# Performance work log

Hardware: AMD Instinct MI355X
Metric: run time of the kernel (lower is better)

Reference implementation:

```python
import jax, jax.numpy as jnp
import numpy as np

ATT_HEAD = 12
IN_DIM = 768
OUT_DIM = IN_DIM // ATT_HEAD
LEAKY_ALPHA = 0.2
B, N = 8, 512


def setup_inputs() -> dict:
    key = jax.random.key(0)
    ks = jax.random.split(key, 8)
    feat_in = jax.random.normal(ks[0], (B, N, IN_DIM), dtype=jnp.float32)
    adj = jax.random.randint(ks[1], (B, N, N), 0, 2) > 0
    # xavier_uniform for W: fan_in=in_dim, fan_out=out_dim
    lim_W = float(np.sqrt(6.0 / (IN_DIM + OUT_DIM)))
    W = jax.random.uniform(ks[2], (ATT_HEAD, IN_DIM, OUT_DIM), minval=-lim_W, maxval=lim_W, dtype=jnp.float32)
    b = jnp.zeros((OUT_DIM,), dtype=jnp.float32)
    lim_w = float(np.sqrt(6.0 / (OUT_DIM + 1)))
    w_src = jax.random.uniform(ks[3], (ATT_HEAD, OUT_DIM, 1), minval=-lim_w, maxval=lim_w, dtype=jnp.float32)
    w_dst = jax.random.uniform(ks[4], (ATT_HEAD, OUT_DIM, 1), minval=-lim_w, maxval=lim_w, dtype=jnp.float32)
    # xavier_normal for H.weight [in_dim, in_dim]
    std_H = float(np.sqrt(2.0 / (IN_DIM + IN_DIM)))
    H_w = jax.random.normal(ks[5], (IN_DIM, IN_DIM), dtype=jnp.float32) * std_H
    H_b = jax.random.normal(ks[6], (IN_DIM,), dtype=jnp.float32) * 0.01
    return {"feat_in": feat_in, "adj": adj, "W": W, "b": b,
            "w_src": w_src, "w_dst": w_dst, "H_w": H_w, "H_b": H_b}


def reference(feat_in, adj, W, b, w_src, w_dst, H_w, H_b):
    # h: [B, heads, N, out_dim]
    h = jnp.einsum('bnd,ade->bane', feat_in, W)
    th = jnp.tanh(h)
    attn_src = jnp.einsum('bane,aeo->bano', th, w_src)  # [B,A,N,1]
    attn_dst = jnp.einsum('bane,aeo->bano', th, w_dst)  # [B,A,N,1]
    attn = attn_src + jnp.swapaxes(attn_dst, 2, 3)      # [B,A,N,N]
    attn = jnp.where(attn >= 0, attn, LEAKY_ALPHA * attn)
    mask = ~adj[:, None, :, :]                           # [B,1,N,N]
    attn = jnp.where(mask, jnp.float32(-999.0), attn)
    attn = jax.nn.softmax(attn, axis=-1)
    feat_out = jnp.einsum('banm,bame->bane', attn, h) + b
    feat_out = jnp.swapaxes(feat_out, 1, 2).reshape(feat_in.shape[0], feat_in.shape[1], -1)
    feat_out = jax.nn.elu(feat_out)
    gate = jax.nn.sigmoid(feat_in @ H_w.T + H_b)
    return gate * feat_out + (1.0 - gate) * feat_in
```

## Files before the change

kernel.cpp:

```cpp
#include <hip/hip_runtime.h>
#include <hip/hip_bf16.h>

#define BB 8
#define NN 512
#define AH 12
#define DIN 768
#define EE 64
#define MM (BB*NN)
#define YY (BB*AH)
#define LEAKY 0.2f

typedef unsigned short u16;
typedef unsigned int u32;
typedef __attribute__((ext_vector_type(8))) short short8;
typedef __attribute__((ext_vector_type(4))) float f32x4;

static __device__ __forceinline__ u16 f2bf(float f) {
    u32 u = __builtin_bit_cast(u32, f);
    u32 r = (u + 0x7FFFu + ((u >> 16) & 1u)) >> 16;
    return (u16)r;
}
static __device__ __forceinline__ u32 pk2(float a, float b) {
    return (u32)f2bf(a) | ((u32)f2bf(b) << 16);
}
static __device__ __forceinline__ float ftanh(float x) {
    x = fminf(fmaxf(x, -15.f), 15.f);
    return 1.f - 2.f / (__expf(2.f * x) + 1.f);
}
static __device__ __forceinline__ void gl_lds16(const u16* g, u16* l) {
    __builtin_amdgcn_global_load_lds((const __attribute__((address_space(1))) unsigned int*)g,
                                     (__attribute__((address_space(3))) unsigned int*)l,
                                     16, 0, 0);
}

static __device__ __forceinline__ void mfma_probe(int lane, int* prow, int* pcol) {
    int q = lane >> 4, x = lane & 15;
    short8 af, bf;
#pragma unroll
    for (int j = 0; j < 8; j++) {
        int k = q * 8 + j;
        af[j] = (short)f2bf((k < 16) ? (float)(x * 16 + k) : 0.f);
        bf[j] = (short)f2bf((k == x) ? 1.f : 0.f);
    }
    f32x4 d = {};
    d = __builtin_amdgcn_mfma_f32_16x16x32_bf16(af, bf, d, 0, 0, 0);
#pragma unroll
    for (int r = 0; r < 4; r++) {
        int v = (int)(d[r] + 0.5f);
        prow[r] = v >> 4;
        pcol[r] = v & 15;
    }
}

__global__ __launch_bounds__(256) void pack_adj_kernel(const int* __restrict__ adj,
                                                       u32* __restrict__ maskbuf) {
    int t = threadIdx.x, w = t >> 6, ln = t & 63;
    int row = blockIdx.x * 4 + w;
    const int* ar = adj + (size_t)row * NN;
#pragma unroll
    for (int it = 0; it < 8; it++) {
        unsigned long long bal = __ballot(ar[it * 64 + ln] != 0);
        if (ln == 0) {
            maskbuf[row * 16 + it * 2]     = (u32)bal;
            maskbuf[row * 16 + it * 2 + 1] = (u32)(bal >> 32);
        }
    }
}

#define N_FEAT (MM*DIN)
#define N_W    (AH*DIN*EE)
__global__ __launch_bounds__(256) void convert_kernel(const float* __restrict__ feat,
                                                      const float* __restrict__ W,
                                                      const float* __restrict__ Hw,
                                                      u16* __restrict__ featb,
                                                      u16* __restrict__ Wt,
                                                      u16* __restrict__ Hwb) {
    int i = blockIdx.x * 256 + threadIdx.x;
    if (i < N_FEAT) { featb[i] = f2bf(feat[i]); return; }
    int i2 = i - N_FEAT;
    if (i2 < N_W) {
        int a = i2 / (DIN * EE), rem = i2 % (DIN * EE);
        int e = rem / DIN, d = rem % DIN;
        Wt[i2] = f2bf(W[a * (DIN * EE) + d * EE + e]);
        return;
    }
    int i3 = i2 - N_W;
    Hwb[i3] = f2bf(Hw[i3]);
}

#define GEMM_CORE(Abase, Bbase)                                               \
    int wm = w & 1, wn = w >> 1, xr = x & 7;                                  \
    int srow = t >> 3;                                                        \
    int skoff = ((t & 7) ^ (srow & 7)) * 8;                                   \
    const u16* Agp = (Abase) + srow * DIN + skoff;                            \
    const u16* Bgp = (Bbase) + srow * DIN + skoff;                            \
    u16* Asw = As + w * 512;                                                  \
    u16* Bsw = Bs + w * 512;                                                  \
    const u16* ApA = As + (wm * 32 + x) * 64;                                 \
    const u16* ApB = Bs + (wn * 32 + x) * 64;                                 \
    f32x4 acc00 = {}, acc01 = {}, acc10 = {}, acc11 = {};                     \
    for (int k0 = 0; k0 < DIN; k0 += 64) {                                    \
        gl_lds16(Agp + k0, Asw);                                              \
        gl_lds16(Agp + 32 * DIN + k0, Asw + 2048);                            \
        gl_lds16(Bgp + k0, Bsw);                                              \
        gl_lds16(Bgp + 32 * DIN + k0, Bsw + 2048);                            \
        __syncthreads();                                                      \
        _Pragma("unroll")                                                     \
        for (int kk = 0; kk < 2; kk++) {                                      \
            int c8 = ((q + kk * 4) ^ xr) * 8;                                 \
            short8 a0 = *(const short8*)(ApA + c8);                           \
            short8 a1 = *(const short8*)(ApA + 16 * 64 + c8);                 \
            short8 b0 = *(const short8*)(ApB + c8);                           \
            short8 b1 = *(const short8*)(ApB + 16 * 64 + c8);                 \
            acc00 = __builtin_amdgcn_mfma_f32_16x16x32_bf16(a0, b0, acc00, 0, 0, 0); \
            acc01 = __builtin_amdgcn_mfma_f32_16x16x32_bf16(a0, b1, acc01, 0, 0, 0); \
            acc10 = __builtin_amdgcn_mfma_f32_16x16x32_bf16(a1, b0, acc10, 0, 0, 0); \
            acc11 = __builtin_amdgcn_mfma_f32_16x16x32_bf16(a1, b1, acc11, 0, 0, 0); \
        }                                                                     \
        __syncthreads();                                                      \
    }                                                                         \
    int prow[4], pcol[4];                                                     \
    mfma_probe(lane, prow, pcol);                                             \
    _Pragma("unroll")                                                         \
    for (int r = 0; r < 4; r++) {                                             \
        cs[wm * 32 + prow[r]][wn * 32 + pcol[r]]           = acc00[r];        \
        cs[wm * 32 + prow[r]][wn * 32 + 16 + pcol[r]]      = acc01[r];        \
        cs[wm * 32 + 16 + prow[r]][wn * 32 + pcol[r]]      = acc10[r];        \
        cs[wm * 32 + 16 + prow[r]][wn * 32 + 16 + pcol[r]] = acc11[r];        \
    }                                                                         \
    __syncthreads();

__global__ __launch_bounds__(256) void gemm_h_kernel(const u16* __restrict__ featb,
                                                     const u16* __restrict__ Wt,
                                                     const float* __restrict__ wsrc,
                                                     const float* __restrict__ wdst,
                                                     u16* __restrict__ hT,
                                                     float* __restrict__ Sbuf,
                                                     float* __restrict__ Dbuf) {
    __shared__ u16 As[64 * 64];
    __shared__ u16 Bs[64 * 64];
    __shared__ alignas(16) float cs[64][68];
    int t = threadIdx.x, w = t >> 6, lane = t & 63, q = lane >> 4, x = lane & 15;
    int m0 = blockIdx.x * 64, a = blockIdx.y;

    GEMM_CORE(featb + (size_t)m0 * DIN, Wt + (size_t)a * EE * DIN)

    int b = m0 >> 9;
    int y = b * AH + a;
    int nbase = m0 & 511;

    {
        int e = t >> 2, ng = t & 3;
        u32* dst = (u32*)&hT[((size_t)y * EE + e) * NN + nbase + ng * 16];
#pragma unroll
        for (int i = 0; i < 8; i++)
            dst[i] = pk2(cs[ng * 16 + 2 * i][e], cs[ng * 16 + 2 * i + 1][e]);
    }
    {
        int r = t >> 2, cg = t & 3;
        float s = 0.f, d = 0.f;
#pragma unroll
        for (int i = 0; i < 16; i++) {
            int e2 = cg * 16 + i;
            float th = ftanh(cs[r][e2]);
            s += th * wsrc[a * EE + e2];
            d += th * wdst[a * EE + e2];
        }
        s += __shfl_xor(s, 1); s += __shfl_xor(s, 2);
        d += __shfl_xor(d, 1); d += __shfl_xor(d, 2);
        if (cg == 0) {
            Sbuf[y * NN + nbase + r] = s;
            Dbuf[y * NN + nbase + r] = d;
        }
    }
}

static __device__ __forceinline__ float sigm(float z) {
    z = fminf(fmaxf(z, -80.f), 80.f);
    return 1.f / (1.f + __expf(-z));
}
__global__ __launch_bounds__(256) void gemm_gate_kernel(const u16* __restrict__ featb,
                                                        const u16* __restrict__ Hwb,
                                                        const float* __restrict__ Hb,
                                                        const float* __restrict__ feat,
                                                        float* __restrict__ out) {
    __shared__ u16 As[64 * 64];
    __shared__ u16 Bs[64 * 64];
    __shared__ alignas(16) float cs[64][68];
    int t = threadIdx.x, w = t >> 6, lane = t & 63, q = lane >> 4, x = lane & 15;
    int m0 = blockIdx.x * 64, n0 = blockIdx.y * 64;

    GEMM_CORE(featb + (size_t)m0 * DIN, Hwb + (size_t)n0 * DIN)

    float4 hb = *(const float4*)&Hb[n0 + (t & 15) * 4];
#pragma unroll
    for (int p = 0; p < 4; p++) {
        int ml = p * 16 + (t >> 4), c4 = (t & 15) * 4;
        float4 v4 = *(const float4*)&cs[ml][c4];
        size_t idx = (size_t)(m0 + ml) * DIN + n0 + c4;
        float4 fo = *(const float4*)&out[idx];
        float4 f4 = *(const float4*)&feat[idx];
        float4 o;
        float g;
        g = sigm(v4.x + hb.x); o.x = g * fo.x + (1.f - g) * f4.x;
        g = sigm(v4.y + hb.y); o.y = g * fo.y + (1.f - g) * f4.y;
        g = sigm(v4.z + hb.z); o.z = g * fo.z + (1.f - g) * f4.z;
        g = sigm(v4.w + hb.w); o.w = g * fo.w + (1.f - g) * f4.w;
        *(float4*)&out[idx] = o;
    }
}

__global__ __launch_bounds__(256) void attn_kernel(const u16* __restrict__ hT,
                                                   const float* __restrict__ Sbuf,
                                                   const float* __restrict__ Dbuf,
                                                   const u32* __restrict__ maskbuf,
                                                   const float* __restrict__ bias,
                                                   float* __restrict__ out) {
    __shared__ alignas(16) float sdst[NN];
    __shared__ u32 smask[64][17];
    __shared__ float silv[64];
    __shared__ alignas(16) float cs[64][68];

    int t = threadIdx.x;
    int y = blockIdx.y, bb = y / AH, a = y % AH;
    int i0 = blockIdx.x * 64;

    sdst[t] = Dbuf[y * NN + t];
    sdst[t + 256] = Dbuf[y * NN + 256 + t];
#pragma unroll
    for (int p = 0; p < 4; p++) {
        int idx = p * 256 + t, r = idx >> 4, c = idx & 15;
        smask[r][c] = maskbuf[((bb << 9) + i0 + r) * 16 + c];
    }
    __syncthreads();

    int w = t >> 6, lane = t & 63, q = lane >> 4, x = lane & 15;
    int rowl = w * 16 + x;
    float srcv = Sbuf[y * NN + i0 + rowl];

    u32 anym = 0;
#pragma unroll
    for (int c = 0; c < 16; c++) anym |= smask[rowl][c];
    int uni = (anym == 0);

    const u16* hTy = hT + (size_t)y * EE * NN;
    f32x4 acc[4] = {};
    float lsum = 0.f;

#pragma unroll 2
    for (int k0 = 0; k0 < NN; k0 += 32) {
        u32 mb = smask[rowl][k0 >> 5] >> (q * 8);
        float pv[8];
#pragma unroll
        for (int j = 0; j < 8; j++) {
            float v = srcv + sdst[k0 + q * 8 + j];
            v = fmaxf(v, LEAKY * v);
            float e = __expf(fminf(v, 60.f));
            float pm = ((mb >> j) & 1) ? e : 0.f;
            pv[j] = uni ? 1.0f : pm;
            lsum += pv[j];
        }
        short8 af;
        af[0] = (short)f2bf(pv[0]); af[1] = (short)f2bf(pv[1]);
        af[2] = (short)f2bf(pv[2]); af[3] = (short)f2bf(pv[3]);
        af[4] = (short)f2bf(pv[4]); af[5] = (short)f2bf(pv[5]);
        af[6] = (short)f2bf(pv[6]); af[7] = (short)f2bf(pv[7]);
        const u16* hp = hTy + (size_t)x * NN + k0 + q * 8;
        short8 b0 = *(const short8*)(hp);
        short8 b1 = *(const short8*)(hp + 16 * NN);
        short8 b2 = *(const short8*)(hp + 32 * NN);
        short8 b3 = *(const short8*)(hp + 48 * NN);
        acc[0] = __builtin_amdgcn_mfma_f32_16x16x32_bf16(af, b0, acc[0], 0, 0, 0);
        acc[1] = __builtin_amdgcn_mfma_f32_16x16x32_bf16(af, b1, acc[1], 0, 0, 0);
        acc[2] = __builtin_amdgcn_mfma_f32_16x16x32_bf16(af, b2, acc[2], 0, 0, 0);
        acc[3] = __builtin_amdgcn_mfma_f32_16x16x32_bf16(af, b3, acc[3], 0, 0, 0);
    }

    lsum += __shfl_xor(lsum, 16);
    lsum += __shfl_xor(lsum, 32);
    if (q == 0) silv[rowl] = 1.f / fmaxf(lsum, 1e-30f);

    int prow[4], pcol[4];
    mfma_probe(lane, prow, pcol);
#pragma unroll
    for (int nt = 0; nt < 4; nt++)
#pragma unroll
        for (int r = 0; r < 4; r++)
            cs[w * 16 + prow[r]][nt * 16 + pcol[r]] = acc[nt][r];
    __syncthreads();

    float4 b4 = *(const float4*)&bias[(t & 15) * 4];
#pragma unroll
    for (int p = 0; p < 4; p++) {
        int nl = p * 16 + (t >> 4), e4 = (t & 15) * 4;
        float il = silv[nl];
        float4 c4 = *(const float4*)&cs[nl][e4];
        float4 o;
        float v;
        v = c4.x * il + b4.x; o.x = v > 0.f ? v : __expf(v) - 1.f;
        v = c4.y * il + b4.y; o.y = v > 0.f ? v : __expf(v) - 1.f;
        v = c4.z * il + b4.z; o.z = v > 0.f ? v : __expf(v) - 1.f;
        v = c4.w * il + b4.w; o.w = v > 0.f ? v : __expf(v) - 1.f;
        *(float4*)&out[((size_t)(bb << 9) + i0 + nl) * DIN + a * EE + e4] = o;
    }
}

extern "C" void kernel_launch(void* const* d_in, const int* in_sizes, int n_in,
                              void* d_out, int out_size, void* d_ws, size_t ws_size,
                              hipStream_t stream) {
    const float* feat  = (const float*)d_in[0];
    const int*   adj   = (const int*)  d_in[1];
    const float* W     = (const float*)d_in[2];
    const float* bvec  = (const float*)d_in[3];
    const float* wsrc  = (const float*)d_in[4];
    const float* wdst  = (const float*)d_in[5];
    const float* Hw    = (const float*)d_in[6];
    const float* Hb    = (const float*)d_in[7];
    float* out = (float*)d_out;

    char* ws = (char*)d_ws;
    u16*  featb   = (u16*)(ws);
    u16*  Wt      = (u16*)(ws + 6291456);
    u16*  Hwb     = (u16*)(ws + 7471104);
    u16*  hT      = (u16*)(ws + 8650752);
    float* Sbuf   = (float*)(ws + 14942208);
    float* Dbuf   = (float*)(ws + 15138816);
    u32*  maskbuf = (u32*)(ws + 15335424);

    pack_adj_kernel<<<MM / 4, 256, 0, stream>>>(adj, maskbuf);
    convert_kernel<<<(N_FEAT + 2 * N_W) / 256, 256, 0, stream>>>(feat, W, Hw, featb, Wt, Hwb);
    gemm_h_kernel<<<dim3(MM / 64, AH), 256, 0, stream>>>(featb, Wt, wsrc, wdst, hT, Sbuf, Dbuf);
    attn_kernel<<<dim3(NN / 64, YY), 256, 0, stream>>>(hT, Sbuf, Dbuf, maskbuf, bvec, out);
    gemm_gate_kernel<<<dim3(MM / 64, DIN / 64), 256, 0, stream>>>(featb, Hwb, Hb, feat, out);
}
```

Measured before the change: 145.3 us.

## Precompute exp factors for leaky-relu softmax and fuse gating into attention epilogue

The src and dst scores are now exponentiated once in the projection kernel as exp(s) and exp(0.2s) pairs. The attention inner loop then forms each weight as a product of two factors, choosing the leaky branch by testing whether the product reaches 1, so no exp is needed per element. BF16 packing of the probabilities switches from rounding to truncation. The gate GEMM now writes sigmoid values to a buffer, and the attention epilogue applies the gated blend with feat, which removes one read-modify-write pass over out. The costs are an extra gate buffer round-trip, clamping of scores to ±40 which can overflow or lose precision for large values, and truncation error in the probabilities.

```diff
diff --git a/kernel.cpp b/kernel.cpp
--- a/kernel.cpp
+++ b/kernel.cpp
@@ -14,6 +14,7 @@
 typedef unsigned int u32;
 typedef __attribute__((ext_vector_type(8))) short short8;
 typedef __attribute__((ext_vector_type(4))) float f32x4;
+typedef __attribute__((ext_vector_type(4))) u32 u32x4;
 
 static __device__ __forceinline__ u16 f2bf(float f) {
     u32 u = __builtin_bit_cast(u32, f);
@@ -22,6 +23,9 @@
 }
 static __device__ __forceinline__ u32 pk2(float a, float b) {
     return (u32)f2bf(a) | ((u32)f2bf(b) << 16);
+}
+static __device__ __forceinline__ u32 pk2t(float a, float b) {
+    return (__builtin_bit_cast(u32, a) >> 16) | (__builtin_bit_cast(u32, b) & 0xFFFF0000u);
 }
 static __device__ __forceinline__ float ftanh(float x) {
     x = fminf(fmaxf(x, -15.f), 15.f);
@@ -135,8 +139,8 @@
                                                      const float* __restrict__ wsrc,
                                                      const float* __restrict__ wdst,
                                                      u16* __restrict__ hT,
-                                                     float* __restrict__ Sbuf,
-                                                     float* __restrict__ Dbuf) {
+                                                     float2* __restrict__ Spair,
+                                                     float2* __restrict__ Dpair) {
     __shared__ u16 As[64 * 64];
     __shared__ u16 Bs[64 * 64];
     __shared__ alignas(16) float cs[64][68];
@@ -169,8 +173,10 @@
         s += __shfl_xor(s, 1); s += __shfl_xor(s, 2);
         d += __shfl_xor(d, 1); d += __shfl_xor(d, 2);
         if (cg == 0) {
-            Sbuf[y * NN + nbase + r] = s;
-            Dbuf[y * NN + nbase + r] = d;
+            s = fminf(fmaxf(s, -40.f), 40.f);
+            d = fminf(fmaxf(d, -40.f), 40.f);
+            Spair[y * NN + nbase + r] = make_float2(__expf(s), __expf(0.2f * s));
+            Dpair[y * NN + nbase + r] = make_float2(__expf(d), __expf(0.2f * d));
         }
     }
 }
@@ -182,8 +188,7 @@
 __global__ __launch_bounds__(256) void gemm_gate_kernel(const u16* __restrict__ featb,
                                                         const u16* __restrict__ Hwb,
                                                         const float* __restrict__ Hb,
-                                                        const float* __restrict__ feat,
-                                                        float* __restrict__ out) {
+                                                        float* __restrict__ Gbuf) {
     __shared__ u16 As[64 * 64];
     __shared__ u16 Bs[64 * 64];
     __shared__ alignas(16) float cs[64][68];
@@ -198,25 +203,24 @@
         int ml = p * 16 + (t >> 4), c4 = (t & 15) * 4;
         float4 v4 = *(const float4*)&cs[ml][c4];
         size_t idx = (size_t)(m0 + ml) * DIN + n0 + c4;
-        float4 fo = *(const float4*)&out[idx];
-        float4 f4 = *(const float4*)&feat[idx];
         float4 o;
-        float g;
-        g = sigm(v4.x + hb.x); o.x = g * fo.x + (1.f - g) * f4.x;
-        g = sigm(v4.y + hb.y); o.y = g * fo.y + (1.f - g) * f4.y;
-        g = sigm(v4.z + hb.z); o.z = g * fo.z + (1.f - g) * f4.z;
-        g = sigm(v4.w + hb.w); o.w = g * fo.w + (1.f - g) * f4.w;
-        *(float4*)&out[idx] = o;
+        o.x = sigm(v4.x + hb.x);
+        o.y = sigm(v4.y + hb.y);
+        o.z = sigm(v4.z + hb.z);
+        o.w = sigm(v4.w + hb.w);
+        *(float4*)&Gbuf[idx] = o;
     }
 }
 
 __global__ __launch_bounds__(256) void attn_kernel(const u16* __restrict__ hT,
-                                                   const float* __restrict__ Sbuf,
-                                                   const float* __restrict__ Dbuf,
+                                                   const float2* __restrict__ Spair,
+                                                   const float2* __restrict__ Dpair,
                                                    const u32* __restrict__ maskbuf,
                                                    const float* __restrict__ bias,
+                                                   const float* __restrict__ Gbuf,
+                                                   const float* __restrict__ feat,
                                                    float* __restrict__ out) {
-    __shared__ alignas(16) float sdst[NN];
+    __shared__ alignas(16) float2 sd2[NN];
     __shared__ u32 smask[64][17];
     __shared__ float silv[64];
     __shared__ alignas(16) float cs[64][68];
@@ -225,8 +229,8 @@
     int y = blockIdx.y, bb = y / AH, a = y % AH;
     int i0 = blockIdx.x * 64;
 
-    sdst[t] = Dbuf[y * NN + t];
-    sdst[t + 256] = Dbuf[y * NN + 256 + t];
+    sd2[t] = Dpair[y * NN + t];
+    sd2[t + 256] = Dpair[y * NN + 256 + t];
 #pragma unroll
     for (int p = 0; p < 4; p++) {
         int idx = p * 256 + t, r = idx >> 4, c = idx & 15;
@@ -236,7 +240,8 @@
 
     int w = t >> 6, lane = t & 63, q = lane >> 4, x = lane & 15;
     int rowl = w * 16 + x;
-    float srcv = Sbuf[y * NN + i0 + rowl];
+    float2 se = Spair[y * NN + i0 + rowl];
+    float es1 = se.x, es2 = se.y;
 
     u32 anym = 0;
 #pragma unroll
@@ -253,18 +258,18 @@
         float pv[8];
 #pragma unroll
         for (int j = 0; j < 8; j++) {
-            float v = srcv + sdst[k0 + q * 8 + j];
-            v = fmaxf(v, LEAKY * v);
-            float e = __expf(fminf(v, 60.f));
-            float pm = ((mb >> j) & 1) ? e : 0.f;
-            pv[j] = uni ? 1.0f : pm;
-            lsum += pv[j];
+            float2 dp = sd2[k0 + q * 8 + j];
+            float m1 = es1 * dp.x;
+            float m2 = es2 * dp.y;
+            float p = (m1 >= 1.f) ? m1 : m2;
+            p = ((mb >> j) & 1) ? p : 0.f;
+            p = uni ? 1.0f : p;
+            lsum += p;
+            pv[j] = p;
         }
-        short8 af;
-        af[0] = (short)f2bf(pv[0]); af[1] = (short)f2bf(pv[1]);
-        af[2] = (short)f2bf(pv[2]); af[3] = (short)f2bf(pv[3]);
-        af[4] = (short)f2bf(pv[4]); af[5] = (short)f2bf(pv[5]);
-        af[6] = (short)f2bf(pv[6]); af[7] = (short)f2bf(pv[7]);
+        short8 af = __builtin_bit_cast(short8, (u32x4){
+            pk2t(pv[0], pv[1]), pk2t(pv[2], pv[3]),
+            pk2t(pv[4], pv[5]), pk2t(pv[6], pv[7])});
         const u16* hp = hTy + (size_t)x * NN + k0 + q * 8;
         short8 b0 = *(const short8*)(hp);
         short8 b1 = *(const short8*)(hp + 16 * NN);
@@ -295,13 +300,16 @@
         int nl = p * 16 + (t >> 4), e4 = (t & 15) * 4;
         float il = silv[nl];
         float4 c4 = *(const float4*)&cs[nl][e4];
+        size_t base = ((size_t)(bb << 9) + i0 + nl) * DIN + a * EE + e4;
+        float4 g4 = *(const float4*)&Gbuf[base];
+        float4 f4 = *(const float4*)&feat[base];
         float4 o;
-        float v;
-        v = c4.x * il + b4.x; o.x = v > 0.f ? v : __expf(v) - 1.f;
-        v = c4.y * il + b4.y; o.y = v > 0.f ? v : __expf(v) - 1.f;
-        v = c4.z * il + b4.z; o.z = v > 0.f ? v : __expf(v) - 1.f;
-        v = c4.w * il + b4.w; o.w = v > 0.f ? v : __expf(v) - 1.f;
-        *(float4*)&out[((size_t)(bb << 9) + i0 + nl) * DIN + a * EE + e4] = o;
+        float v, e;
+        v = c4.x * il + b4.x; e = v > 0.f ? v : __expf(v) - 1.f; o.x = g4.x * e + (1.f - g4.x) * f4.x;
+        v = c4.y * il + b4.y; e = v > 0.f ? v : __expf(v) - 1.f; o.y = g4.y * e + (1.f - g4.y) * f4.y;
+        v = c4.z * il + b4.z; e = v > 0.f ? v : __expf(v) - 1.f; o.z = g4.z * e + (1.f - g4.z) * f4.z;
+        v = c4.w * il + b4.w; e = v > 0.f ? v : __expf(v) - 1.f; o.w = g4.w * e + (1.f - g4.w) * f4.w;
+        *(float4*)&out[base] = o;
     }
 }
 
@@ -319,17 +327,18 @@
     float* out = (float*)d_out;
 
     char* ws = (char*)d_ws;
-    u16*  featb   = (u16*)(ws);
-    u16*  Wt      = (u16*)(ws + 6291456);
-    u16*  Hwb     = (u16*)(ws + 7471104);
-    u16*  hT      = (u16*)(ws + 8650752);
-    float* Sbuf   = (float*)(ws + 14942208);
-    float* Dbuf   = (float*)(ws + 15138816);
-    u32*  maskbuf = (u32*)(ws + 15335424);
+    u16*    featb   = (u16*)(ws);
+    u16*    Wt      = (u16*)(ws + 6291456);
+    u16*    Hwb     = (u16*)(ws + 7471104);
+    u16*    hT      = (u16*)(ws + 8650752);
+    float2* Spair   = (float2*)(ws + 14942208);
+    float2* Dpair   = (float2*)(ws + 15335424);
+    u32*    maskbuf = (u32*)(ws + 15728640);
+    float*  Gbuf    = (float*)(ws + 15990784);
 
     pack_adj_kernel<<<MM / 4, 256, 0, stream>>>(adj, maskbuf);
     convert_kernel<<<(N_FEAT + 2 * N_W) / 256, 256, 0, stream>>>(feat, W, Hw, featb, Wt, Hwb);
-    gemm_h_kernel<<<dim3(MM / 64, AH), 256, 0, stream>>>(featb, Wt, wsrc, wdst, hT, Sbuf, Dbuf);
-    attn_kernel<<<dim3(NN / 64, YY), 256, 0, stream>>>(hT, Sbuf, Dbuf, maskbuf, bvec, out);
-    gemm_gate_kernel<<<dim3(MM / 64, DIN / 64), 256, 0, stream>>>(featb, Hwb, Hb, feat, out);
-}
+    gemm_h_kernel<<<dim3(MM / 64, AH), 256, 0, stream>>>(featb, Wt, wsrc, wdst, hT, Spair, Dpair);
+    gemm_gate_kernel<<<dim3(MM / 64, DIN / 64), 256, 0, stream>>>(featb, Hwb, Hb, Gbuf);
+    attn_kernel<<<dim3(NN / 64, YY), 256, 0, stream>>>(hT, Spair, Dpair, maskbuf, bvec, Gbuf, feat, out);
+}
```

Result: no change. 142.6 us (-1.9%).
